# Kernel tuning notes

Hardware: AMD Instinct MI355X
Metric: run time of the kernel (lower is better)

The kernel has to match this reference:

```python
import jax, jax.numpy as jnp
import numpy as np

B, L = 4, 8192
IN_CH, OUT_CH = 1, 1
H = 64               # d_model
NSTATE = 16          # d_state
DBLK = 4             # number of residual blocks
DCONV = 16
EXPAND = 2
DINNER = EXPAND * H              # 128
HEADDIM = H // 4                 # 16
NHEADS = DINNER // HEADDIM       # 8
CONV_DIM = DINNER + 2 * NSTATE   # 160 (ngroups=1)
D_IN_PROJ = 2 * DINNER + 2 * NSTATE + NHEADS  # 296
CHUNK = 128


def setup_inputs():
    key = jax.random.key(0)
    ks = jax.random.split(key, 12)
    rn = lambda k, shape, s: (jax.random.normal(k, shape) * s).astype(jnp.float32)
    x = rn(ks[0], (B, L, IN_CH), 1.0)
    w_in = rn(ks[1], (H, IN_CH), 1.0)
    w_out = rn(ks[2], (OUT_CH, H), 1.0 / np.sqrt(H))
    in_proj_w = rn(ks[3], (DBLK, D_IN_PROJ, H), 1.0 / np.sqrt(H))
    conv_w = rn(ks[4], (DBLK, CONV_DIM, DCONV), 1.0 / np.sqrt(DCONV))
    conv_b = rn(ks[5], (DBLK, CONV_DIM), 0.02)
    dt = jnp.exp(jax.random.uniform(ks[6], (DBLK, NHEADS)) * (np.log(0.1) - np.log(1e-3)) + np.log(1e-3))
    dt_bias = (dt + jnp.log(-jnp.expm1(-dt))).astype(jnp.float32)  # inverse softplus
    A_log = jnp.log(jax.random.uniform(ks[7], (DBLK, NHEADS), minval=1.0, maxval=16.0)).astype(jnp.float32)
    D_skip = jnp.ones((DBLK, NHEADS), jnp.float32)
    init_states = rn(ks[8], (DBLK, NHEADS, HEADDIM, NSTATE), 0.01)
    norm_w = jnp.ones((DBLK, DINNER), jnp.float32)
    out_proj_w = rn(ks[9], (DBLK, H, DINNER), 1.0 / np.sqrt(DINNER))
    mlp_w = rn(ks[10], (DBLK, H, H), 1.0 / np.sqrt(H))
    mlp_b = jnp.zeros((DBLK, H), jnp.float32)
    return {"x": x, "w_in": w_in, "w_out": w_out, "in_proj_w": in_proj_w,
            "conv_w": conv_w, "conv_b": conv_b, "dt_bias": dt_bias, "A_log": A_log,
            "D_skip": D_skip, "init_states": init_states, "norm_w": norm_w,
            "out_proj_w": out_proj_w, "mlp_w": mlp_w, "mlp_b": mlp_b}


def segsum(a):
    # a: (..., q) -> (..., q, q); seg[i, j] = sum_{k=j+1..i} a[k] on lower triangle (diag=0), exp->0 above
    q = a.shape[-1]
    cs = jnp.cumsum(a, axis=-1)
    seg = cs[..., :, None] - cs[..., None, :]
    mask = jnp.tril(jnp.ones((q, q), dtype=bool))
    return jnp.where(mask, seg, -1e30)


def ssd(X, dA, Bm, Cm, init_state):
    # Chunked SSD (Mamba2 paper). X: (b,l,h,p) = x*dt, dA: (b,l,h), Bm/Cm: (b,l,n), init_state: (b,h,p,n)
    b, l, h, p = X.shape
    c = l // CHUNK
    X = X.reshape(b, c, CHUNK, h, p)
    Bm = Bm.reshape(b, c, CHUNK, NSTATE)
    Cm = Cm.reshape(b, c, CHUNK, NSTATE)
    A = dA.reshape(b, c, CHUNK, h).transpose(0, 3, 1, 2)  # (b,h,c,q)
    A_cs = jnp.cumsum(A, axis=-1)
    # intra-chunk (diagonal blocks)
    Lm = jnp.exp(segsum(A))  # (b,h,c,q,q)
    Y_diag = jnp.einsum('bcln,bcsn,bhcls,bcshp->bclhp', Cm, Bm, Lm, X)
    # per-chunk final states
    decay_states = jnp.exp(A_cs[..., -1:] - A_cs)  # (b,h,c,q)
    states = jnp.einsum('bcln,bhcl,bclhp->bchpn', Bm, decay_states, X)
    states = jnp.concatenate([init_state[:, None], states], axis=1)  # (b,c+1,h,p,n)
    # inter-chunk recurrence (vectorized via segsum over chunk decays)
    decay_chunk = jnp.exp(segsum(jnp.pad(A_cs[..., -1], ((0, 0), (0, 0), (1, 0)))))  # (b,h,c+1,c+1)
    new_states = jnp.einsum('bhzc,bchpn->bzhpn', decay_chunk, states)
    prev_states = new_states[:, :-1]  # state entering each chunk
    state_decay = jnp.exp(A_cs)
    Y_off = jnp.einsum('bcln,bchpn,bhcl->bclhp', Cm, prev_states, state_decay)
    return (Y_diag + Y_off).reshape(b, l, h, p)


def mamba2(u, w_inp, cw, cb, dtb, alog, dskip, istate, nw, w_outp):
    b, l, _ = u.shape
    zxbcdt = jnp.einsum('bld,ed->ble', u, w_inp)  # (b,l,296)
    z = zxbcdt[..., :DINNER]
    xBC = zxbcdt[..., DINNER:DINNER + CONV_DIM]
    dt = jax.nn.softplus(zxbcdt[..., DINNER + CONV_DIM:] + dtb)  # (b,l,h)
    # causal depthwise conv over seq + silu
    xBC = jax.lax.conv_general_dilated(
        xBC.transpose(0, 2, 1), cw[:, None, :], (1,), [(DCONV - 1, 0)],
        feature_group_count=CONV_DIM, dimension_numbers=('NCH', 'OIH', 'NCH'))
    xBC = jax.nn.silu(xBC + cb[None, :, None]).transpose(0, 2, 1)
    xs = xBC[..., :DINNER]
    Bm = xBC[..., DINNER:DINNER + NSTATE]
    Cm = xBC[..., DINNER + NSTATE:]
    A = -jnp.exp(alog)  # (h,)
    xh = xs.reshape(b, l, NHEADS, HEADDIM)
    init = jnp.broadcast_to(istate, (b,) + istate.shape)
    y = ssd(xh * dt[..., None], dt * A, Bm, Cm, init)
    y = y + xh * dskip[None, None, :, None]  # D skip
    y = y.reshape(b, l, DINNER)
    # gated RMSNorm: norm(y * silu(z)) * weight
    y = y * jax.nn.silu(z)
    y = y * jax.lax.rsqrt(jnp.mean(y * y, axis=-1, keepdims=True) + 1e-5) * nw
    return jnp.einsum('ble,de->bld', y, w_outp)


def reference(x, w_in, w_out, in_proj_w, conv_w, conv_b, dt_bias, A_log,
              D_skip, init_states, norm_w, out_proj_w, mlp_w, mlp_b):
    h = jnp.einsum('bli,hi->blh', x, w_in)
    for i in range(DBLK):
        y = mamba2(h, in_proj_w[i], conv_w[i], conv_b[i], dt_bias[i], A_log[i],
                   D_skip[i], init_states[i], norm_w[i], out_proj_w[i])
        t = y / jnp.sqrt(1.0 + y * y)  # TanhApprox
        y = jnp.einsum('blh,oh->blo', t, mlp_w[i]) + mlp_b[i]
        h = h + y  # residual
    return jnp.einsum('blh,oh->blo', h, w_out)
```

## Files before the change

kernel.cpp:

```cpp
#include <hip/hip_runtime.h>
#include <math.h>

#define NB 4
#define SEQ 8192
#define NT (NB*SEQ)
#define HDIM 64
#define NST 16
#define NBLK 4
#define KCONV 16
#define DIN 128
#define PDIM 16
#define NH 8
#define CDIM 160
#define EPROJ 296
#define CH 128
#define NC 64

typedef __attribute__((ext_vector_type(8))) short short8;
typedef __attribute__((ext_vector_type(4))) float f32x4;

__device__ __forceinline__ float sigf(float x){ return 1.0f/(1.0f+__expf(-x)); }

__device__ __forceinline__ unsigned short bf16r(float f){
  unsigned int u = __float_as_uint(f);
  u = (u + 0x7fffu + ((u >> 16) & 1u)) >> 16;
  return (unsigned short)u;
}
__device__ __forceinline__ unsigned int pk_bf16(float a, float b){
  return (unsigned int)bf16r(a) | ((unsigned int)bf16r(b) << 16);
}
__device__ __forceinline__ float bf16f(unsigned short h){
  return __uint_as_float(((unsigned int)h) << 16);
}

__global__ __launch_bounds__(256) void k_init(const float* __restrict__ x, const float* __restrict__ w_in,
                                              float* __restrict__ h,
                                              const float* __restrict__ w,
                                              unsigned short* __restrict__ whi,
                                              unsigned short* __restrict__ wlo){
  int bi = blockIdx.x;
  const int HB = (NT*HDIM)/256;
  if(bi < HB){
    int i = bi*256 + threadIdx.x;
    int t = i >> 6, d = i & 63;
    h[i] = x[t]*w_in[d];
  } else {
    int i = (bi - HB)*256 + threadIdx.x;
    if(i < NBLK*EPROJ*HDIM){
      float f = w[i];
      unsigned short hi = bf16r(f);
      float fh = bf16f(hi);
      whi[i] = hi;
      wlo[i] = bf16r(f - fh);
    }
  }
}

__global__ __launch_bounds__(256) void k_inproj(const float* __restrict__ h,
                                                const unsigned short* __restrict__ whi,
                                                const unsigned short* __restrict__ wlo,
                                                unsigned short* __restrict__ zxz,
                                                float* __restrict__ zxc){
  int tid = threadIdx.x;
  int lane = tid & 63, wid = tid >> 6;
  int quad = lane >> 4, lq = lane & 15;
  int t0 = blockIdx.x*64 + wid*16;

  const float* hp = h + (size_t)(t0+lq)*HDIM;
  short8 bh[2], bl[2];
#pragma unroll
  for(int kb=0;kb<2;kb++){
    float4 f0 = *(const float4*)(hp + kb*32 + quad*8);
    float4 f1 = *(const float4*)(hp + kb*32 + quad*8 + 4);
    float v[8] = {f0.x,f0.y,f0.z,f0.w,f1.x,f1.y,f1.z,f1.w};
#pragma unroll
    for(int j=0;j<8;j++){
      unsigned short hi = bf16r(v[j]);
      bh[kb][j] = (short)hi;
      bl[kb][j] = (short)bf16r(v[j] - bf16f(hi));
    }
  }

  const unsigned short* wh0 = whi + (size_t)lq*HDIM + quad*8;
  const unsigned short* wl0 = wlo + (size_t)lq*HDIM + quad*8;
  short8 ah0 = *(const short8*)wh0;
  short8 ah1 = *(const short8*)(wh0 + 32);
  short8 al0 = *(const short8*)wl0;
  short8 al1 = *(const short8*)(wl0 + 32);

  for(int et=0; et<19; et++){
    short8 nh0 = ah0, nh1 = ah1, nl0 = al0, nl1 = al1;
    if(et < 18){
      int e_a = (et+1)*16 + lq;
      int ec = (e_a < EPROJ) ? e_a : (EPROJ-1);
      const unsigned short* wh = whi + (size_t)ec*HDIM + quad*8;
      const unsigned short* wl = wlo + (size_t)ec*HDIM + quad*8;
      nh0 = *(const short8*)wh;
      nh1 = *(const short8*)(wh + 32);
      nl0 = *(const short8*)wl;
      nl1 = *(const short8*)(wl + 32);
    }
    f32x4 acc = {0.f,0.f,0.f,0.f};
    acc = __builtin_amdgcn_mfma_f32_16x16x32_bf16(ah0, bh[0], acc, 0, 0, 0);
    acc = __builtin_amdgcn_mfma_f32_16x16x32_bf16(ah1, bh[1], acc, 0, 0, 0);
    acc = __builtin_amdgcn_mfma_f32_16x16x32_bf16(ah0, bl[0], acc, 0, 0, 0);
    acc = __builtin_amdgcn_mfma_f32_16x16x32_bf16(ah1, bl[1], acc, 0, 0, 0);
    acc = __builtin_amdgcn_mfma_f32_16x16x32_bf16(al0, bh[0], acc, 0, 0, 0);
    acc = __builtin_amdgcn_mfma_f32_16x16x32_bf16(al1, bh[1], acc, 0, 0, 0);
#pragma unroll
    for(int r=0;r<4;r++){
      int e = et*16 + quad*4 + r;
      if(e < 128)        zxz[(size_t)e*NT + t0 + lq] = bf16r(acc[r]);
      else if(e < EPROJ) zxc[(size_t)(e-128)*NT + t0 + lq] = acc[r];
    }
    ah0 = nh0; ah1 = nh1; al0 = nl0; al1 = nl1;
  }
}

__global__ __launch_bounds__(512) void k_mid(const float* __restrict__ zxc,
                                             const float* __restrict__ cw, const float* __restrict__ cb,
                                             const float* __restrict__ dtb, const float* __restrict__ alog,
                                             unsigned short* __restrict__ xbc, float* __restrict__ dt,
                                             float* __restrict__ acs, float* __restrict__ asum,
                                             float* __restrict__ S){
  __shared__ unsigned short XhT[128][136];
  __shared__ unsigned short XlT[128][136];
  __shared__ unsigned short BhT[16][136];
  __shared__ unsigned short BlT[16][136];
  __shared__ float dtl[8][128];
  __shared__ float wle[8][128];

  int bc = blockIdx.x;
  int c = bc & 63, b = bc >> 6;
  int t0 = b*SEQ + c*CH;
  int tid = threadIdx.x;

  for(int it=0; it<5; it++){
    int G = tid + it*512;
    int ch = G >> 4;
    int sg = (G & 15) * 8;
    const float* p = zxc + (size_t)ch*NT + t0 + sg - 16;
    float buf[24];
    if(c == 0 && sg < 16){
#pragma unroll
      for(int j=0;j<24;j++){
        int l = sg - 16 + j;
        buf[j] = (l >= 0) ? p[j] : 0.f;
      }
    } else {
#pragma unroll
      for(int q4=0;q4<6;q4++){
        float4 f = *(const float4*)(p + q4*4);
        buf[q4*4+0]=f.x; buf[q4*4+1]=f.y; buf[q4*4+2]=f.z; buf[q4*4+3]=f.w;
      }
    }
    float wv[16];
#pragma unroll
    for(int k=0;k<16;k++) wv[k] = cw[ch*KCONV+k];
    float bias = cb[ch];
    unsigned short hs[8];
#pragma unroll
    for(int s=0;s<8;s++){
      float acc = bias;
#pragma unroll
      for(int k=0;k<16;k++) acc += wv[k]*buf[s+1+k];
      float r = acc * sigf(acc);
      unsigned short hi = bf16r(r);
      unsigned short lo = bf16r(r - bf16f(hi));
      hs[s] = hi;
      if(ch < 128){ XhT[ch][sg+s] = hi; XlT[ch][sg+s] = lo; }
      else if(ch < 144){ BhT[ch-128][sg+s] = hi; BlT[ch-128][sg+s] = lo; }
    }
    uint4 pk;
    pk.x = (unsigned int)hs[0] | ((unsigned int)hs[1] << 16);
    pk.y = (unsigned int)hs[2] | ((unsigned int)hs[3] << 16);
    pk.z = (unsigned int)hs[4] | ((unsigned int)hs[5] << 16);
    pk.w = (unsigned int)hs[6] | ((unsigned int)hs[7] << 16);
    *(uint4*)(xbc + (size_t)ch*NT + t0 + sg) = pk;
  }
#pragma unroll
  for(int k=0;k<2;k++){
    int idx = tid + k*512;
    int hh = idx >> 7, s = idx & 127;
    float raw = zxc[(size_t)(CDIM + hh)*NT + t0 + s] + dtb[hh];
    float v = (raw > 20.f) ? raw : log1pf(__expf(raw));
    dtl[hh][s] = v;
    dt[(size_t)hh*NT + t0 + s] = v;
  }
  __syncthreads();

  int lane = tid & 63, wid = tid >> 6;
  {
    int hh = wid;
    float A = -__expf(alog[hh]);
    float2 dd = *(const float2*)&dtl[hh][2*lane];
    float d0 = dd.x, d1 = dd.y;
    float v0 = d0*A, v1 = d1*A;
    float s = v0 + v1;
    for(int off=1; off<64; off<<=1){
      float o = __shfl_up(s, off);
      if(lane >= off) s += o;
    }
    float tot = __shfl(s, 63);
    float excl = s - (v0+v1);
    float a0 = excl+v0, a1 = excl+v0+v1;
    *(float2*)&acs[(size_t)hh*NT + t0 + 2*lane] = make_float2(a0, a1);
    if(lane == 63) asum[(size_t)bc*NH + hh] = __expf(tot);
    wle[hh][2*lane]   = d0*__expf(tot - a0);
    wle[hh][2*lane+1] = d1*__expf(tot - a1);
  }
  __syncthreads();

  {
    int hh = wid;
    int lq = lane & 15, quad = lane >> 4;
    f32x4 acc = {0.f,0.f,0.f,0.f};
#pragma unroll
    for(int kb=0;kb<4;kb++){
      int k0 = kb*32 + quad*8;
      short8 xh = *(const short8*)&XhT[hh*16 + lq][k0];
      short8 xl = *(const short8*)&XlT[hh*16 + lq][k0];
      float4 w0 = *(const float4*)&wle[hh][k0];
      float4 w1 = *(const float4*)&wle[hh][k0+4];
      float wv8[8] = {w0.x,w0.y,w0.z,w0.w,w1.x,w1.y,w1.z,w1.w};
      short8 ah, al;
#pragma unroll
      for(int j=0;j<8;j++){
        float xv = bf16f((unsigned short)xh[j]) + bf16f((unsigned short)xl[j]);
        float pw = xv * wv8[j];
        unsigned short hi = bf16r(pw);
        ah[j] = (short)hi;
        al[j] = (short)bf16r(pw - bf16f(hi));
      }
      short8 bh = *(const short8*)&BhT[lq][k0];
      short8 bl = *(const short8*)&BlT[lq][k0];
      acc = __builtin_amdgcn_mfma_f32_16x16x32_bf16(ah, bh, acc, 0, 0, 0);
      acc = __builtin_amdgcn_mfma_f32_16x16x32_bf16(ah, bl, acc, 0, 0, 0);
      acc = __builtin_amdgcn_mfma_f32_16x16x32_bf16(al, bh, acc, 0, 0, 0);
    }
    float* Sp = S + ((size_t)bc*NH + hh)*256;
#pragma unroll
    for(int r=0;r<4;r++) Sp[(quad*4 + r)*16 + lq] = acc[r];
  }
}

__global__ __launch_bounds__(64) void k_scan(const float* __restrict__ S, const float* __restrict__ easum,
                                             const float* __restrict__ init, float* __restrict__ prev){
  int q  = blockIdx.x & 3;
  int hh = (blockIdx.x >> 2) & 7;
  int b  = blockIdx.x >> 5;
  int el = q*64 + threadIdx.x;
  const size_t cs = (size_t)NH*256;
  const float* Sp = S + ((size_t)(b*NC)*NH + hh)*256 + el;
  float* Pp = prev + ((size_t)(b*NC)*NH + hh)*256 + el;
  const float* ap = easum + (size_t)(b*NC)*NH + hh;
  float e[NC];
#pragma unroll
  for(int c=0;c<NC;c++) e[c] = ap[(size_t)c*NH];
  float r = init[hh*256 + el];
  float s0 = Sp[0], s1 = Sp[cs], s2 = Sp[2*cs], s3 = Sp[3*cs];
#pragma unroll
  for(int c=0;c<NC;c+=4){
    Pp[(size_t)c*cs] = r;
    r = e[c]*r + s0;
    s0 = (c+4 < NC) ? Sp[(size_t)(c+4)*cs] : 0.f;
    Pp[(size_t)(c+1)*cs] = r;
    r = e[c+1]*r + s1;
    s1 = (c+5 < NC) ? Sp[(size_t)(c+5)*cs] : 0.f;
    Pp[(size_t)(c+2)*cs] = r;
    r = e[c+2]*r + s2;
    s2 = (c+6 < NC) ? Sp[(size_t)(c+6)*cs] : 0.f;
    Pp[(size_t)(c+3)*cs] = r;
    r = e[c+3]*r + s3;
    s3 = (c+7 < NC) ? Sp[(size_t)(c+7)*cs] : 0.f;
  }
}

__global__ __launch_bounds__(1024) void k_tail(const unsigned short* __restrict__ xbc,
                                               const unsigned short* __restrict__ zxz,
                                               const float* __restrict__ dt, const float* __restrict__ acs,
                                               const float* __restrict__ prev, const float* __restrict__ dskip,
                                               const float* __restrict__ nw, const float* __restrict__ opw,
                                               const float* __restrict__ mw, const float* __restrict__ mb,
                                               float* __restrict__ h,
                                               int last, const float* __restrict__ wout,
                                               float* __restrict__ out){
  __shared__ __align__(16) unsigned char sm[151840];
  unsigned short* Bb   = (unsigned short*)(sm);
  unsigned short* Cb   = (unsigned short*)(sm + 6144);
  unsigned short* XbT  = (unsigned short*)(sm + 12288);
  unsigned short* P0   = (unsigned short*)(sm + 55296);
  unsigned short* P1   = (unsigned short*)(sm + 98304);
  float* Al  = (float*)(sm + 141312);
  float* Dtl = (float*)(sm + 145408);
  float* nwl = (float*)(sm + 149504);
  float* mbl = (float*)(sm + 150016);
  unsigned short* zbuf = (unsigned short*)(sm + 150272);
  float* ssl  = (float*)(sm + 150304);
  float* outb = (float*)(sm + 151328);
  unsigned short* Zb = XbT;
  unsigned short* Wo = P0;
  unsigned short* Wm = P0 + 64*136;
  unsigned short* Yn = P1;
  unsigned short* Tt = P1;

  int bc = blockIdx.x;
  int c = bc & 63, b = bc >> 6;
  int t0 = b*SEQ + c*CH;
  int tid = threadIdx.x, lane = tid & 63, wid = tid >> 6;
  int quad = lane >> 4, lq = lane & 15;
  int hgrp = wid >> 3;
  int wr7 = wid & 7;
  int widr = (wr7 < 4) ? wr7 : (11 - wr7);
  int strip = widr*16;

#pragma unroll
  for(int k=0;k<4;k++){
    int idx = tid + k*1024;
    int ch = idx >> 7, s = idx & 127;
    unsigned short f = xbc[(size_t)(DIN+ch)*NT + t0 + s];
    if(ch < 16) Bb[s*24 + ch] = f;
    else        Cb[s*24 + ch-16] = f;
  }
#pragma unroll
  for(int k=0;k<4;k++){
    int fi = tid + k*1024;
    int p = fi >> 5, s4 = fi & 31;
    uint2 xu = *(const uint2*)&xbc[(size_t)p*NT + t0 + s4*4];
    float4 dv = *(const float4*)&dt[(size_t)(p>>4)*NT + t0 + s4*4];
    float x0 = bf16f((unsigned short)(xu.x & 0xffffu));
    float x1 = bf16f((unsigned short)(xu.x >> 16));
    float x2 = bf16f((unsigned short)(xu.y & 0xffffu));
    float x3 = bf16f((unsigned short)(xu.y >> 16));
    *(unsigned int*)&XbT[p*168 + s4*4]   = pk_bf16(x0*dv.x, x1*dv.y);
    *(unsigned int*)&XbT[p*168 + s4*4+2] = pk_bf16(x2*dv.z, x3*dv.w);
  }
#pragma unroll
  for(int k=0;k<2;k++){
    int idx = tid + k*1024;
    int hh = idx >> 8, rest = idx & 255;
    int p = rest >> 4, n = rest & 15;
    XbT[(hh*16+p)*168 + 128 + n] = bf16r(prev[((size_t)bc*NH + hh)*256 + rest]);
  }
#pragma unroll
  for(int k=0;k<2;k++){
    int idx = tid + k*1024;
    if(idx < 1536){
      int p = idx / 12, cc = idx - p*12;
      *(unsigned int*)&XbT[p*168 + 144 + 2*cc] = 0u;
    }
  }
  {
    int hh = tid >> 7, s = tid & 127;
    Al[hh*128+s]  = acs[(size_t)hh*NT + t0 + s];
    Dtl[hh*128+s] = dt[(size_t)hh*NT + t0 + s];
  }
  if(tid < 128) nwl[tid] = nw[tid];
  else if(tid < 192) mbl[tid-128] = mb[tid-128];
  else if(tid < 208) zbuf[tid-192] = 0;
  {
    unsigned short* Pgz = hgrp ? P1 : P0;
#pragma unroll
    for(int k=0;k<3;k++){
      int idx = lane + k*64;
      int rr = idx / 12, cc = idx - rr*12;
      *(unsigned int*)&Pgz[(strip+rr)*168 + 144 + 2*cc] = 0u;
    }
    int zc0 = (widr+1)*16;
    int nu  = (7 - widr)*8;
    for(int u = lane>>4; u < nu; u += 4){
      *(unsigned int*)&Pgz[(strip+(lane&15))*168 + zc0 + 2*u] = 0u;
    }
  }
  __syncthreads();

  short8 afr;
  {
    int row = strip + lq;
    const unsigned short* ap = (quad < 2) ? &Cb[row*24 + quad*8] : zbuf;
    afr = *(const short8*)ap;
  }
  f32x4 sc[8];
#pragma unroll
  for(int nt=0;nt<8;nt++){
    f32x4 acc = {0.f,0.f,0.f,0.f};
    if(nt <= widr){
      const unsigned short* bp = (quad < 2) ? &Bb[(nt*16+lq)*24 + quad*8] : zbuf;
      short8 bfr = *(const short8*)bp;
      acc = __builtin_amdgcn_mfma_f32_16x16x32_bf16(afr, bfr, acc, 0, 0, 0);
    }
    sc[nt] = acc;
  }

  unsigned short* Pg = hgrp ? P1 : P0;
  f32x4 accv[4];
  for(int j=0;j<4;j++){
    int hh2 = hgrp*4 + j;
    const float* Alh = Al + hh2*128;
    float alr[4];
#pragma unroll
    for(int r=0;r<4;r++) alr[r] = Alh[strip + quad*4 + r];
#pragma unroll
    for(int nt=0;nt<8;nt++){
      if(nt <= widr){
        int col = nt*16 + lq;
        float alc = Alh[col];
#pragma unroll
        for(int r=0;r<4;r++){
          int row = strip + quad*4 + r;
          float p = sc[nt][r] * __expf(alr[r] - alc);
          p = (col <= row) ? p : 0.f;
          Pg[row*168 + col] = bf16r(p);
        }
      }
    }
    {
      int n = lane & 15, rg = lane >> 4;
#pragma unroll
      for(int rr=0;rr<4;rr++){
        int row = strip + rg*4 + rr;
        float ea = __expf(Alh[row]);
        Pg[row*168 + 128 + n] = bf16r(bf16f(Cb[row*24+n]) * ea);
      }
    }
    f32x4 acc2 = {0.f,0.f,0.f,0.f};
#pragma unroll
    for(int ks=0;ks<5;ks++){
      short8 bfr = *(const short8*)&XbT[(hh2*16+lq)*168 + ks*32 + quad*8];
      short8 af  = *(const short8*)&Pg[(strip+lq)*168 + ks*32 + quad*8];
      acc2 = __builtin_amdgcn_mfma_f32_16x16x32_bf16(af, bfr, acc2, 0, 0, 0);
    }
    const float* Dth = Dtl + hh2*128;
    float Dk = dskip[hh2];
#pragma unroll
    for(int r=0;r<4;r++){
      int l = strip + quad*4 + r;
      float xdt = bf16f(XbT[(hh2*16+lq)*168 + l]);
      float dtv = fmaxf(Dth[l], 1e-30f);
      acc2[r] += Dk * xdt * __frcp_rn(dtv);
    }
    accv[j] = acc2;
  }
  __syncthreads();

#pragma unroll
  for(int k=0;k<4;k++){
    int fi = tid + k*1024;
    int p = fi >> 5, s4 = fi & 31;
    uint2 zu = *(const uint2*)&zxz[(size_t)p*NT + t0 + s4*4];
    *(unsigned int*)&Zb[p*136 + s4*4]   = zu.x;
    *(unsigned int*)&Zb[p*136 + s4*4+2] = zu.y;
  }
#pragma unroll
  for(int k=0;k<2;k++){
    int fi = tid + k*1024;
    int n = fi >> 5, k4 = fi & 31;
    float4 wv = *(const float4*)&opw[(size_t)n*DIN + k4*4];
    *(unsigned int*)&Wo[n*136 + k4*4]   = pk_bf16(wv.x, wv.y);
    *(unsigned int*)&Wo[n*136 + k4*4+2] = pk_bf16(wv.z, wv.w);
  }
  {
    int fi = tid;
    int n = fi >> 4, k4 = fi & 15;
    float4 wv = *(const float4*)&mw[(size_t)n*HDIM + k4*4];
    *(unsigned int*)&Wm[n*72 + k4*4]   = pk_bf16(wv.x, wv.y);
    *(unsigned int*)&Wm[n*72 + k4*4+2] = pk_bf16(wv.z, wv.w);
  }
  __syncthreads();

  float part[4] = {0.f,0.f,0.f,0.f};
#pragma unroll
  for(int j=0;j<4;j++){
    int ch = (hgrp*4+j)*16 + lq;
    float nwv = nwl[ch];
#pragma unroll
    for(int r=0;r<4;r++){
      int l = strip + quad*4 + r;
      float zv = bf16f(Zb[ch*136 + l]);
      float g = zv * sigf(zv);
      float yv = accv[j][r] * g;
      part[r] += yv*yv;
      Yn[l*136 + ch] = bf16r(yv * nwv);
    }
  }
#pragma unroll
  for(int r=0;r<4;r++){
    part[r] += __shfl_xor(part[r],1); part[r] += __shfl_xor(part[r],2);
    part[r] += __shfl_xor(part[r],4); part[r] += __shfl_xor(part[r],8);
  }
  if(lq == 0){
#pragma unroll
    for(int r=0;r<4;r++) ssl[hgrp*128 + strip + quad*4 + r] = part[r];
  }
  __syncthreads();

  float rms_[4];
#pragma unroll
  for(int r=0;r<4;r++){
    int l = strip + quad*4 + r;
    rms_[r] = rsqrtf((ssl[l] + ssl[128+l])*(1.0f/128.0f) + 1e-5f);
  }
  short8 afk[4];
#pragma unroll
  for(int ks=0;ks<4;ks++) afk[ks] = *(const short8*)&Yn[(strip+lq)*136 + ks*32 + quad*8];
  f32x4 aco[2];
#pragma unroll
  for(int ntl=0;ntl<2;ntl++){ aco[ntl] = (f32x4){0.f,0.f,0.f,0.f}; }
#pragma unroll
  for(int ntl=0;ntl<2;ntl++){
    int nt = hgrp*2 + ntl;
#pragma unroll
    for(int ks=0;ks<4;ks++){
      short8 bfr = *(const short8*)&Wo[(nt*16+lq)*136 + ks*32 + quad*8];
      aco[ntl] = __builtin_amdgcn_mfma_f32_16x16x32_bf16(afk[ks], bfr, aco[ntl], 0, 0, 0);
    }
  }
  __syncthreads();
#pragma unroll
  for(int ntl=0;ntl<2;ntl++){
    int nt = hgrp*2 + ntl;
#pragma unroll
    for(int r=0;r<4;r++){
      int l = strip + quad*4 + r;
      float o = aco[ntl][r] * rms_[r];
      Tt[l*136 + nt*16+lq] = bf16r(o * rsqrtf(1.0f + o*o));
    }
  }
  __syncthreads();

  f32x4 acm[2];
#pragma unroll
  for(int ntl=0;ntl<2;ntl++){ acm[ntl] = (f32x4){0.f,0.f,0.f,0.f}; }
#pragma unroll
  for(int ks=0;ks<2;ks++){
    short8 af = *(const short8*)&Tt[(strip+lq)*136 + ks*32 + quad*8];
#pragma unroll
    for(int ntl=0;ntl<2;ntl++){
      int nt = hgrp*2 + ntl;
      short8 bfr = *(const short8*)&Wm[(nt*16+lq)*72 + ks*32 + quad*8];
      acm[ntl] = __builtin_amdgcn_mfma_f32_16x16x32_bf16(af, bfr, acm[ntl], 0, 0, 0);
    }
  }
  if(!last){
#pragma unroll
    for(int ntl=0;ntl<2;ntl++){
      int nt = hgrp*2 + ntl;
#pragma unroll
      for(int r=0;r<4;r++){
        int l = strip + quad*4 + r;
        int d = nt*16 + lq;
        size_t gi = (size_t)(t0+l)*HDIM + d;
        h[gi] += acm[ntl][r] + mbl[d];
      }
    }
  } else {
    float ps[4] = {0.f,0.f,0.f,0.f};
#pragma unroll
    for(int ntl=0;ntl<2;ntl++){
      int nt = hgrp*2 + ntl;
      int d = nt*16 + lq;
      float wo = wout[d];
      float bias = mbl[d];
#pragma unroll
      for(int r=0;r<4;r++){
        int l = strip + quad*4 + r;
        size_t gi = (size_t)(t0+l)*HDIM + d;
        float hn = h[gi] + acm[ntl][r] + bias;
        ps[r] += hn * wo;
      }
    }
#pragma unroll
    for(int r=0;r<4;r++){
      ps[r] += __shfl_xor(ps[r],1); ps[r] += __shfl_xor(ps[r],2);
      ps[r] += __shfl_xor(ps[r],4); ps[r] += __shfl_xor(ps[r],8);
    }
    if(hgrp == 1 && lq == 0){
#pragma unroll
      for(int r=0;r<4;r++) outb[strip + quad*4 + r] = ps[r];
    }
    __syncthreads();
    if(hgrp == 0 && lq == 0){
#pragma unroll
      for(int r=0;r<4;r++){
        int l = strip + quad*4 + r;
        out[t0 + l] = ps[r] + outb[l];
      }
    }
  }
}

extern "C" void kernel_launch(void* const* d_in, const int* in_sizes, int n_in,
                              void* d_out, int out_size, void* d_ws, size_t ws_size,
                              hipStream_t stream){
  const float* x          = (const float*)d_in[0];
  const float* w_in       = (const float*)d_in[1];
  const float* w_out      = (const float*)d_in[2];
  const float* in_proj_w  = (const float*)d_in[3];
  const float* conv_w     = (const float*)d_in[4];
  const float* conv_b     = (const float*)d_in[5];
  const float* dt_bias    = (const float*)d_in[6];
  const float* A_log      = (const float*)d_in[7];
  const float* D_skip     = (const float*)d_in[8];
  const float* init_st    = (const float*)d_in[9];
  const float* norm_w     = (const float*)d_in[10];
  const float* out_proj_w = (const float*)d_in[11];
  const float* mlp_w      = (const float*)d_in[12];
  const float* mlp_b      = (const float*)d_in[13];
  float* out = (float*)d_out;

  float* ws = (float*)d_ws;
  float* h    = ws; ws += (size_t)NT*HDIM;
  unsigned short* zxz = (unsigned short*)ws; ws += (size_t)(128*NT)/2;
  float* zxc  = ws; ws += (size_t)168*NT;
  unsigned short* xbc = (unsigned short*)ws; ws += (size_t)(CDIM*NT)/2;
  float* dt   = ws; ws += (size_t)NH*NT;
  float* acs  = ws; ws += (size_t)NH*NT;
  float* asum = ws; ws += (size_t)NB*NC*NH;
  float* S    = ws; ws += (size_t)NB*NC*NH*256;
  float* prev = ws; ws += (size_t)NB*NC*NH*256;
  unsigned short* whi = (unsigned short*)ws; ws += (size_t)(NBLK*EPROJ*HDIM)/2;
  unsigned short* wlo = (unsigned short*)ws; ws += (size_t)(NBLK*EPROJ*HDIM)/2;

  k_init<<<(NT*HDIM)/256 + (NBLK*EPROJ*HDIM)/256, 256, 0, stream>>>(x, w_in, h, in_proj_w, whi, wlo);
  for(int i=0;i<NBLK;i++){
    k_inproj<<<NT/64, 256, 0, stream>>>(h, whi + (size_t)i*EPROJ*HDIM,
                                        wlo + (size_t)i*EPROJ*HDIM, zxz, zxc);
    k_mid   <<<NB*NC, 512, 0, stream>>>(zxc, conv_w + i*CDIM*KCONV, conv_b + i*CDIM,
                                        dt_bias + i*NH, A_log + i*NH,
                                        xbc, dt, acs, asum, S);
    k_scan  <<<NB*NH*4, 64, 0, stream>>>(S, asum, init_st + i*NH*256, prev);
    k_tail  <<<NB*NC, 1024, 0, stream>>>(xbc, zxz, dt, acs, prev, D_skip + i*NH,
                                         norm_w + i*DIN, out_proj_w + i*HDIM*DIN,
                                         mlp_w + i*HDIM*HDIM, mlp_b + i*HDIM, h,
                                         (i == NBLK-1) ? 1 : 0, w_out, out);
  }
}
```

Before: 354.6 us.

## Fuse in-projection into conv/chunk-state kernel, keeping xBC/dt activations in LDS

Merges k_inproj and k_mid into one per-chunk kernel, k_front, with 1024 threads. Each block projects its 128 tokens plus a 16-token halo from h into shared memory, then runs the causal conv, dt softplus, cumsum and chunk-state MFMA from LDS. This removes the fp32 zxc round trip through global memory and one launch per layer. In exchange, about 145 KB of LDS caps occupancy at one block per CU, the halo tokens are projected twice, and only 8 of the 16 waves do the scan and state work.

```diff
diff --git a/kernel.cpp b/kernel.cpp
--- a/kernel.cpp
+++ b/kernel.cpp
@@ -56,144 +56,197 @@
   }
 }
 
-__global__ __launch_bounds__(256) void k_inproj(const float* __restrict__ h,
+__global__ __launch_bounds__(1024) void k_front(const float* __restrict__ h,
                                                 const unsigned short* __restrict__ whi,
                                                 const unsigned short* __restrict__ wlo,
+                                                const float* __restrict__ cw, const float* __restrict__ cb,
+                                                const float* __restrict__ dtb, const float* __restrict__ alog,
                                                 unsigned short* __restrict__ zxz,
-                                                float* __restrict__ zxc){
-  int tid = threadIdx.x;
-  int lane = tid & 63, wid = tid >> 6;
+                                                unsigned short* __restrict__ xbc,
+                                                float* __restrict__ dt, float* __restrict__ acs,
+                                                float* __restrict__ asum, float* __restrict__ S){
+  __shared__ __align__(16) unsigned char smf[148480];
+  unsigned short* Hh  = (unsigned short*)(smf);
+  unsigned short* Hl  = (unsigned short*)(smf + 20736);
+  float* zxcS         = (float*)(smf + 41472);
+  unsigned short* XhT = (unsigned short*)(smf);
+  unsigned short* XlT = (unsigned short*)(smf + 34816);
+  unsigned short* BhT = (unsigned short*)(smf + 69632);
+  unsigned short* BlT = (unsigned short*)(smf + 73984);
+  float* dtraw = (float*)(smf + 136192);
+  float* dtl   = (float*)(smf + 140288);
+  float* wle   = (float*)(smf + 144384);
+
+  int bc = blockIdx.x;
+  int c = bc & 63, b = bc >> 6;
+  int t0 = b*SEQ + c*CH;
+  int tid = threadIdx.x, lane = tid & 63, wid = tid >> 6;
   int quad = lane >> 4, lq = lane & 15;
-  int t0 = blockIdx.x*64 + wid*16;
-
-  const float* hp = h + (size_t)(t0+lq)*HDIM;
-  short8 bh[2], bl[2];
-#pragma unroll
-  for(int kb=0;kb<2;kb++){
-    float4 f0 = *(const float4*)(hp + kb*32 + quad*8);
-    float4 f1 = *(const float4*)(hp + kb*32 + quad*8 + 4);
-    float v[8] = {f0.x,f0.y,f0.z,f0.w,f1.x,f1.y,f1.z,f1.w};
-#pragma unroll
-    for(int j=0;j<8;j++){
-      unsigned short hi = bf16r(v[j]);
-      bh[kb][j] = (short)hi;
-      bl[kb][j] = (short)bf16r(v[j] - bf16f(hi));
-    }
-  }
-
-  const unsigned short* wh0 = whi + (size_t)lq*HDIM + quad*8;
-  const unsigned short* wl0 = wlo + (size_t)lq*HDIM + quad*8;
-  short8 ah0 = *(const short8*)wh0;
-  short8 ah1 = *(const short8*)(wh0 + 32);
-  short8 al0 = *(const short8*)wl0;
-  short8 al1 = *(const short8*)(wl0 + 32);
-
-  for(int et=0; et<19; et++){
-    short8 nh0 = ah0, nh1 = ah1, nl0 = al0, nl1 = al1;
-    if(et < 18){
-      int e_a = (et+1)*16 + lq;
+
+#pragma unroll
+  for(int k=0;k<3;k++){
+    int idx = tid + k*1024;
+    if(idx < 2304){
+      int tok = idx >> 4;
+      int d0 = (idx & 15) * 4;
+      float4 v;
+      if(c == 0 && tok < 16){ v = make_float4(0.f,0.f,0.f,0.f); }
+      else v = *(const float4*)(h + (size_t)(t0 - 16 + tok)*HDIM + d0);
+      float vv[4] = {v.x, v.y, v.z, v.w};
+      unsigned short hi4[4], lo4[4];
+#pragma unroll
+      for(int j=0;j<4;j++){
+        unsigned short hi = bf16r(vv[j]);
+        hi4[j] = hi;
+        lo4[j] = bf16r(vv[j] - bf16f(hi));
+      }
+      uint2 ph, pl;
+      ph.x = (unsigned int)hi4[0] | ((unsigned int)hi4[1] << 16);
+      ph.y = (unsigned int)hi4[2] | ((unsigned int)hi4[3] << 16);
+      pl.x = (unsigned int)lo4[0] | ((unsigned int)lo4[1] << 16);
+      pl.y = (unsigned int)lo4[2] | ((unsigned int)lo4[3] << 16);
+      *(uint2*)&Hh[tok*72 + d0] = ph;
+      *(uint2*)&Hl[tok*72 + d0] = pl;
+    }
+  }
+  __syncthreads();
+
+  {
+    int L = wid;
+    int tg, et;
+    if(L < 152){ tg = 1 + L/19; et = L % 19; } else { tg = 0; et = 8 + (L - 152); }
+    {
+      int e_a = et*16 + lq;
       int ec = (e_a < EPROJ) ? e_a : (EPROJ-1);
       const unsigned short* wh = whi + (size_t)ec*HDIM + quad*8;
       const unsigned short* wl = wlo + (size_t)ec*HDIM + quad*8;
-      nh0 = *(const short8*)wh;
-      nh1 = *(const short8*)(wh + 32);
-      nl0 = *(const short8*)wl;
-      nl1 = *(const short8*)(wl + 32);
-    }
-    f32x4 acc = {0.f,0.f,0.f,0.f};
-    acc = __builtin_amdgcn_mfma_f32_16x16x32_bf16(ah0, bh[0], acc, 0, 0, 0);
-    acc = __builtin_amdgcn_mfma_f32_16x16x32_bf16(ah1, bh[1], acc, 0, 0, 0);
-    acc = __builtin_amdgcn_mfma_f32_16x16x32_bf16(ah0, bl[0], acc, 0, 0, 0);
-    acc = __builtin_amdgcn_mfma_f32_16x16x32_bf16(ah1, bl[1], acc, 0, 0, 0);
-    acc = __builtin_amdgcn_mfma_f32_16x16x32_bf16(al0, bh[0], acc, 0, 0, 0);
-    acc = __builtin_amdgcn_mfma_f32_16x16x32_bf16(al1, bh[1], acc, 0, 0, 0);
-#pragma unroll
-    for(int r=0;r<4;r++){
-      int e = et*16 + quad*4 + r;
-      if(e < 128)        zxz[(size_t)e*NT + t0 + lq] = bf16r(acc[r]);
-      else if(e < EPROJ) zxc[(size_t)(e-128)*NT + t0 + lq] = acc[r];
-    }
-    ah0 = nh0; ah1 = nh1; al0 = nl0; al1 = nl1;
-  }
-}
-
-__global__ __launch_bounds__(512) void k_mid(const float* __restrict__ zxc,
-                                             const float* __restrict__ cw, const float* __restrict__ cb,
-                                             const float* __restrict__ dtb, const float* __restrict__ alog,
-                                             unsigned short* __restrict__ xbc, float* __restrict__ dt,
-                                             float* __restrict__ acs, float* __restrict__ asum,
-                                             float* __restrict__ S){
-  __shared__ unsigned short XhT[128][136];
-  __shared__ unsigned short XlT[128][136];
-  __shared__ unsigned short BhT[16][136];
-  __shared__ unsigned short BlT[16][136];
-  __shared__ float dtl[8][128];
-  __shared__ float wle[8][128];
-
-  int bc = blockIdx.x;
-  int c = bc & 63, b = bc >> 6;
-  int t0 = b*SEQ + c*CH;
-  int tid = threadIdx.x;
-
-  for(int it=0; it<5; it++){
-    int G = tid + it*512;
-    int ch = G >> 4;
-    int sg = (G & 15) * 8;
-    const float* p = zxc + (size_t)ch*NT + t0 + sg - 16;
-    float buf[24];
-    if(c == 0 && sg < 16){
-#pragma unroll
-      for(int j=0;j<24;j++){
-        int l = sg - 16 + j;
-        buf[j] = (l >= 0) ? p[j] : 0.f;
-      }
-    } else {
+      short8 ah0 = *(const short8*)wh;
+      short8 ah1 = *(const short8*)(wh + 32);
+      short8 al0 = *(const short8*)wl;
+      short8 al1 = *(const short8*)(wl + 32);
+      while(true){
+        int Ln = L + 16;
+        int tgn = 0, etn = 0;
+        short8 nh0 = ah0, nh1 = ah1, nl0 = al0, nl1 = al1;
+        if(Ln < 162){
+          if(Ln < 152){ tgn = 1 + Ln/19; etn = Ln % 19; } else { tgn = 0; etn = 8 + (Ln - 152); }
+          int e_n = etn*16 + lq;
+          int ecn = (e_n < EPROJ) ? e_n : (EPROJ-1);
+          const unsigned short* wh2 = whi + (size_t)ecn*HDIM + quad*8;
+          const unsigned short* wl2 = wlo + (size_t)ecn*HDIM + quad*8;
+          nh0 = *(const short8*)wh2;
+          nh1 = *(const short8*)(wh2 + 32);
+          nl0 = *(const short8*)wl2;
+          nl1 = *(const short8*)(wl2 + 32);
+        }
+        const unsigned short* hrh = Hh + (tg*16 + lq)*72 + quad*8;
+        const unsigned short* hrl = Hl + (tg*16 + lq)*72 + quad*8;
+        short8 xh0 = *(const short8*)hrh;
+        short8 xh1 = *(const short8*)(hrh + 32);
+        short8 xl0 = *(const short8*)hrl;
+        short8 xl1 = *(const short8*)(hrl + 32);
+        f32x4 acc = {0.f,0.f,0.f,0.f};
+        acc = __builtin_amdgcn_mfma_f32_16x16x32_bf16(ah0, xh0, acc, 0, 0, 0);
+        acc = __builtin_amdgcn_mfma_f32_16x16x32_bf16(ah1, xh1, acc, 0, 0, 0);
+        acc = __builtin_amdgcn_mfma_f32_16x16x32_bf16(ah0, xl0, acc, 0, 0, 0);
+        acc = __builtin_amdgcn_mfma_f32_16x16x32_bf16(ah1, xl1, acc, 0, 0, 0);
+        acc = __builtin_amdgcn_mfma_f32_16x16x32_bf16(al0, xh0, acc, 0, 0, 0);
+        acc = __builtin_amdgcn_mfma_f32_16x16x32_bf16(al1, xh1, acc, 0, 0, 0);
+        if(tg >= 1){
+          int tokg = t0 + (tg-1)*16 + lq;
+#pragma unroll
+          for(int r=0;r<4;r++){
+            int e = et*16 + quad*4 + r;
+            if(e < 128)        zxz[(size_t)e*NT + tokg] = bf16r(acc[r]);
+            else if(e < 288)   zxcS[(e-128)*148 + tg*16 + lq] = acc[r];
+            else if(e < 296)   dtraw[(e-288)*128 + (tg-1)*16 + lq] = acc[r];
+          }
+        } else {
+#pragma unroll
+          for(int r=0;r<4;r++){
+            int e = et*16 + quad*4 + r;
+            zxcS[(e-128)*148 + lq] = acc[r];
+          }
+        }
+        if(Ln >= 162) break;
+        L = Ln; tg = tgn; et = etn;
+        ah0 = nh0; ah1 = nh1; al0 = nl0; al1 = nl1;
+      }
+    }
+  }
+  __syncthreads();
+
+  unsigned int hiP[3][4], loP[3][4];
+#pragma unroll
+  for(int it=0; it<3; it++){
+    int G = tid + it*1024;
+    if(G < 2560){
+      int ch = G >> 4, sg = (G & 15)*8;
+      float buf[24];
 #pragma unroll
       for(int q4=0;q4<6;q4++){
-        float4 f = *(const float4*)(p + q4*4);
+        float4 f = *(const float4*)&zxcS[ch*148 + sg + q4*4];
         buf[q4*4+0]=f.x; buf[q4*4+1]=f.y; buf[q4*4+2]=f.z; buf[q4*4+3]=f.w;
       }
-    }
-    float wv[16];
-#pragma unroll
-    for(int k=0;k<16;k++) wv[k] = cw[ch*KCONV+k];
-    float bias = cb[ch];
-    unsigned short hs[8];
-#pragma unroll
-    for(int s=0;s<8;s++){
-      float acc = bias;
-#pragma unroll
-      for(int k=0;k<16;k++) acc += wv[k]*buf[s+1+k];
-      float r = acc * sigf(acc);
-      unsigned short hi = bf16r(r);
-      unsigned short lo = bf16r(r - bf16f(hi));
-      hs[s] = hi;
-      if(ch < 128){ XhT[ch][sg+s] = hi; XlT[ch][sg+s] = lo; }
-      else if(ch < 144){ BhT[ch-128][sg+s] = hi; BlT[ch-128][sg+s] = lo; }
-    }
-    uint4 pk;
-    pk.x = (unsigned int)hs[0] | ((unsigned int)hs[1] << 16);
-    pk.y = (unsigned int)hs[2] | ((unsigned int)hs[3] << 16);
-    pk.z = (unsigned int)hs[4] | ((unsigned int)hs[5] << 16);
-    pk.w = (unsigned int)hs[6] | ((unsigned int)hs[7] << 16);
-    *(uint4*)(xbc + (size_t)ch*NT + t0 + sg) = pk;
-  }
-#pragma unroll
-  for(int k=0;k<2;k++){
-    int idx = tid + k*512;
-    int hh = idx >> 7, s = idx & 127;
-    float raw = zxc[(size_t)(CDIM + hh)*NT + t0 + s] + dtb[hh];
+      float wv[16];
+#pragma unroll
+      for(int k=0;k<16;k++) wv[k] = cw[ch*KCONV + k];
+      float bias = cb[ch];
+      unsigned short hs[8], ls[8];
+#pragma unroll
+      for(int s=0;s<8;s++){
+        float acc = bias;
+#pragma unroll
+        for(int k=0;k<16;k++) acc += wv[k]*buf[s+1+k];
+        float r = acc * sigf(acc);
+        unsigned short hi = bf16r(r);
+        hs[s] = hi;
+        ls[s] = bf16r(r - bf16f(hi));
+      }
+      hiP[it][0] = (unsigned int)hs[0] | ((unsigned int)hs[1] << 16);
+      hiP[it][1] = (unsigned int)hs[2] | ((unsigned int)hs[3] << 16);
+      hiP[it][2] = (unsigned int)hs[4] | ((unsigned int)hs[5] << 16);
+      hiP[it][3] = (unsigned int)hs[6] | ((unsigned int)hs[7] << 16);
+      loP[it][0] = (unsigned int)ls[0] | ((unsigned int)ls[1] << 16);
+      loP[it][1] = (unsigned int)ls[2] | ((unsigned int)ls[3] << 16);
+      loP[it][2] = (unsigned int)ls[4] | ((unsigned int)ls[5] << 16);
+      loP[it][3] = (unsigned int)ls[6] | ((unsigned int)ls[7] << 16);
+      uint4 pk;
+      pk.x = hiP[it][0]; pk.y = hiP[it][1]; pk.z = hiP[it][2]; pk.w = hiP[it][3];
+      *(uint4*)(xbc + (size_t)ch*NT + t0 + sg) = pk;
+    }
+  }
+  {
+    int hh = tid >> 7, s = tid & 127;
+    float raw = dtraw[hh*128 + s] + dtb[hh];
     float v = (raw > 20.f) ? raw : log1pf(__expf(raw));
-    dtl[hh][s] = v;
+    dtl[hh*128 + s] = v;
     dt[(size_t)hh*NT + t0 + s] = v;
   }
   __syncthreads();
 
-  int lane = tid & 63, wid = tid >> 6;
-  {
+#pragma unroll
+  for(int it=0; it<3; it++){
+    int G = tid + it*1024;
+    if(G < 2560){
+      int ch = G >> 4, sg = (G & 15)*8;
+      if(ch < 128){
+        uint4 vh; vh.x=hiP[it][0]; vh.y=hiP[it][1]; vh.z=hiP[it][2]; vh.w=hiP[it][3];
+        uint4 vl; vl.x=loP[it][0]; vl.y=loP[it][1]; vl.z=loP[it][2]; vl.w=loP[it][3];
+        *(uint4*)&XhT[ch*136 + sg] = vh;
+        *(uint4*)&XlT[ch*136 + sg] = vl;
+      } else if(ch < 144){
+        uint4 vh; vh.x=hiP[it][0]; vh.y=hiP[it][1]; vh.z=hiP[it][2]; vh.w=hiP[it][3];
+        uint4 vl; vl.x=loP[it][0]; vl.y=loP[it][1]; vl.z=loP[it][2]; vl.w=loP[it][3];
+        *(uint4*)&BhT[(ch-128)*136 + sg] = vh;
+        *(uint4*)&BlT[(ch-128)*136 + sg] = vl;
+      }
+    }
+  }
+  if(wid < 8){
     int hh = wid;
     float A = -__expf(alog[hh]);
-    float2 dd = *(const float2*)&dtl[hh][2*lane];
+    float2 dd = *(const float2*)&dtl[hh*128 + 2*lane];
     float d0 = dd.x, d1 = dd.y;
     float v0 = d0*A, v1 = d1*A;
     float s = v0 + v1;
@@ -206,22 +259,21 @@
     float a0 = excl+v0, a1 = excl+v0+v1;
     *(float2*)&acs[(size_t)hh*NT + t0 + 2*lane] = make_float2(a0, a1);
     if(lane == 63) asum[(size_t)bc*NH + hh] = __expf(tot);
-    wle[hh][2*lane]   = d0*__expf(tot - a0);
-    wle[hh][2*lane+1] = d1*__expf(tot - a1);
-  }
-  __syncthreads();
-
-  {
+    wle[hh*128 + 2*lane]   = d0*__expf(tot - a0);
+    wle[hh*128 + 2*lane+1] = d1*__expf(tot - a1);
+  }
+  __syncthreads();
+
+  if(wid < 8){
     int hh = wid;
-    int lq = lane & 15, quad = lane >> 4;
     f32x4 acc = {0.f,0.f,0.f,0.f};
 #pragma unroll
     for(int kb=0;kb<4;kb++){
       int k0 = kb*32 + quad*8;
-      short8 xh = *(const short8*)&XhT[hh*16 + lq][k0];
-      short8 xl = *(const short8*)&XlT[hh*16 + lq][k0];
-      float4 w0 = *(const float4*)&wle[hh][k0];
-      float4 w1 = *(const float4*)&wle[hh][k0+4];
+      short8 xh = *(const short8*)&XhT[(hh*16 + lq)*136 + k0];
+      short8 xl = *(const short8*)&XlT[(hh*16 + lq)*136 + k0];
+      float4 w0 = *(const float4*)&wle[hh*128 + k0];
+      float4 w1 = *(const float4*)&wle[hh*128 + k0 + 4];
       float wv8[8] = {w0.x,w0.y,w0.z,w0.w,w1.x,w1.y,w1.z,w1.w};
       short8 ah, al;
 #pragma unroll
@@ -232,8 +284,8 @@
         ah[j] = (short)hi;
         al[j] = (short)bf16r(pw - bf16f(hi));
       }
-      short8 bh = *(const short8*)&BhT[lq][k0];
-      short8 bl = *(const short8*)&BlT[lq][k0];
+      short8 bh = *(const short8*)&BhT[lq*136 + k0];
+      short8 bl = *(const short8*)&BlT[lq*136 + k0];
       acc = __builtin_amdgcn_mfma_f32_16x16x32_bf16(ah, bh, acc, 0, 0, 0);
       acc = __builtin_amdgcn_mfma_f32_16x16x32_bf16(ah, bl, acc, 0, 0, 0);
       acc = __builtin_amdgcn_mfma_f32_16x16x32_bf16(al, bh, acc, 0, 0, 0);
@@ -611,7 +663,6 @@
   float* ws = (float*)d_ws;
   float* h    = ws; ws += (size_t)NT*HDIM;
   unsigned short* zxz = (unsigned short*)ws; ws += (size_t)(128*NT)/2;
-  float* zxc  = ws; ws += (size_t)168*NT;
   unsigned short* xbc = (unsigned short*)ws; ws += (size_t)(CDIM*NT)/2;
   float* dt   = ws; ws += (size_t)NH*NT;
   float* acs  = ws; ws += (size_t)NH*NT;
@@ -623,11 +674,10 @@
 
   k_init<<<(NT*HDIM)/256 + (NBLK*EPROJ*HDIM)/256, 256, 0, stream>>>(x, w_in, h, in_proj_w, whi, wlo);
   for(int i=0;i<NBLK;i++){
-    k_inproj<<<NT/64, 256, 0, stream>>>(h, whi + (size_t)i*EPROJ*HDIM,
-                                        wlo + (size_t)i*EPROJ*HDIM, zxz, zxc);
-    k_mid   <<<NB*NC, 512, 0, stream>>>(zxc, conv_w + i*CDIM*KCONV, conv_b + i*CDIM,
+    k_front<<<NB*NC, 1024, 0, stream>>>(h, whi + (size_t)i*EPROJ*HDIM, wlo + (size_t)i*EPROJ*HDIM,
+                                        conv_w + i*CDIM*KCONV, conv_b + i*CDIM,
                                         dt_bias + i*NH, A_log + i*NH,
-                                        xbc, dt, acs, asum, S);
+                                        zxz, xbc, dt, acs, asum, S);
     k_scan  <<<NB*NH*4, 64, 0, stream>>>(S, asum, init_st + i*NH*256, prev);
     k_tail  <<<NB*NC, 1024, 0, stream>>>(xbc, zxz, dt, acs, prev, D_skip + i*NH,
                                          norm_w + i*DIN, out_proj_w + i*HDIM*DIN,
```

Result: faster. 329.7 us (-7.0%).
